# Optimization experiments

Hardware: AMD Instinct MI355X
Metric: run time of the kernel (lower is better)

Reference implementation:

```python
import jax, jax.numpy as jnp
import numpy as np

B, S, D, H, C, L, V, MLP, OUT = 2, 1024, 512, 8, 64, 1, 32000, 1024, 32000
DH = D // H
ROT = DH // 2  # RotaryEmbedding(dim=emb_dim//(2*n_heads)) -> rotates first d_head/2 dims
EPS = 1e-5
THETA = 10000.0


def layer_norm(x, g, b):
    m = x.mean(-1, keepdims=True)
    v = ((x - m) ** 2).mean(-1, keepdims=True)
    return (x - m) / jnp.sqrt(v + EPS) * g + b


def apply_rope(k):
    # k: (B, H, S, DH); interleaved-pair rotary on first ROT dims (rotary_embedding_torch)
    s = k.shape[-2]
    inv = 1.0 / (THETA ** (jnp.arange(0, ROT, 2, dtype=jnp.float32) / ROT))  # (ROT//2,)
    ang = jnp.arange(s, dtype=jnp.float32)[:, None] * inv[None, :]          # (S, ROT//2)
    ang = jnp.repeat(ang, 2, axis=-1)                                       # (S, ROT) interleaved
    cos, sin = jnp.cos(ang), jnp.sin(ang)
    kr = k[..., :ROT]
    k1, k2 = kr[..., 0::2], kr[..., 1::2]
    rot = jnp.stack([-k2, k1], axis=-1).reshape(kr.shape)
    kr = kr * cos + rot * sin
    return jnp.concatenate([kr, k[..., ROT:]], axis=-1)


def compression_attention(x, q_down, Wq, bq, Wk, bk, Wv, bv, Wo, bo):
    # x: (B, S, D) -- batch_first, causal branch, dropout=0 (eval)
    b_, s, d = x.shape
    qu = x @ Wq + bq
    kd = x @ Wk + bk
    vd = x @ Wv + bv
    vdk = vd @ Wk + bk
    vdv = vd @ Wv + bv
    split = lambda t: t.reshape(b_, s, H, DH).transpose(0, 2, 1, 3)  # (B,H,S,DH)
    qu, kd, vdk, vdv = map(split, (qu, kd, vdk, vdv))
    qd = q_down.reshape(C, H, DH).transpose(1, 0, 2)                 # (H,C,DH)
    kd = apply_rope(kd)
    scale = DH ** -0.5
    down = jnp.einsum('hcd,bhsd->bhcs', qd * scale, kd)              # (B,H,C,S)
    w = jnp.exp(down - down.max(-1, keepdims=True))
    norm = jnp.cumsum(w, axis=-1)                                    # (B,H,C,S)
    vkv = jnp.concatenate([vdk, vdv], axis=-1)                       # (B,H,S,2DH)
    # running compressed K/V state: (B,H,C,S,2DH)
    kvu = jnp.cumsum(w[..., None] * vkv[:, :, None, :, :], axis=3) / norm[..., None]
    ku, vu = kvu[..., :DH], kvu[..., DH:]
    up = jnp.einsum('bhsd,bhcsd->bhsc', qu * scale, ku)
    up = jax.nn.softmax(up, axis=-1)
    out = jnp.einsum('bhsc,bhcsd->bhsd', up, vu)
    out = out.transpose(0, 2, 1, 3).reshape(b_, s, d)
    return out @ Wo + bo


def setup_inputs():
    key = jax.random.key(0)
    ks = jax.random.split(key, 16)
    g = lambda i, shape, sc=0.02: jax.random.normal(ks[i], shape, jnp.float32) * sc
    return {
        'tokens': jax.random.randint(ks[0], (B, S), 0, V, dtype=jnp.int32),
        'emb': g(1, (V, D)),
        'ln1_g': jnp.ones((L, D), jnp.float32), 'ln1_b': jnp.zeros((L, D), jnp.float32),
        'q_down': g(2, (L, C, D)),
        'Wq': g(3, (L, D, D)), 'bq': jnp.zeros((L, D), jnp.float32),
        'Wk': g(4, (L, D, D)), 'bk': jnp.zeros((L, D), jnp.float32),
        'Wv': g(5, (L, D, D)), 'bv': jnp.zeros((L, D), jnp.float32),
        'Wo': g(6, (L, D, D)), 'bo': jnp.zeros((L, D), jnp.float32),
        'ln2_g': jnp.ones((L, D), jnp.float32), 'ln2_b': jnp.zeros((L, D), jnp.float32),
        'W1': g(7, (L, D, MLP)), 'b1': jnp.zeros((L, MLP), jnp.float32),
        'W2': g(8, (L, MLP, D)), 'b2': jnp.zeros((L, D), jnp.float32),
        'lnf_g': jnp.ones((D,), jnp.float32), 'lnf_b': jnp.zeros((D,), jnp.float32),
        'Wout': g(9, (D, OUT)),
    }


def reference(tokens, emb, ln1_g, ln1_b, q_down, Wq, bq, Wk, bk, Wv, bv, Wo, bo,
              ln2_g, ln2_b, W1, b1, W2, b2, lnf_g, lnf_b, Wout):
    x = emb[tokens]  # (B,S,D)
    for l in range(L):
        h = layer_norm(x, ln1_g[l], ln1_b[l])
        a = compression_attention(h, q_down[l], Wq[l], bq[l], Wk[l], bk[l],
                                  Wv[l], bv[l], Wo[l], bo[l])
        # NOTE: original code residual-adds to the *normed* x (x was reassigned)
        x = layer_norm(h + a, ln2_g[l], ln2_b[l])
        ff = jax.nn.relu(x @ W1[l] + b1[l]) @ W2[l] + b2[l]
        x = x + ff
    x = layer_norm(x, lnf_g, lnf_b)
    return x @ Wout  # (B,S,OUT)
```

## Files before the change

### kernel.cpp

```cpp
#include <hip/hip_runtime.h>
#include <hip/hip_bf16.h>
#include <cstdint>

typedef unsigned short u16;
typedef unsigned int u32;
typedef __bf16 bf16_t;
typedef bf16_t bf16x8 __attribute__((ext_vector_type(8)));
typedef float f32x4 __attribute__((ext_vector_type(4)));

constexpr int Bn = 2, Sn = 1024, Dn = 512, Hn = 8, Cn = 64, DHn = 64, ROTn = 32;
constexpr int MLPn = 1024, OUTn = 32000;
constexpr int NCH = 32;
constexpr int CSs = Sn / NCH;
constexpr float SCALE = 0.125f;
constexpr float EPSf = 1e-5f;
constexpr int QKVW = 1536;
constexpr int KVW = 1024;

__device__ __forceinline__ u16 f2b(float x) {
  u32 u = __float_as_uint(x);
  u32 r = (u + 0x7FFFu + ((u >> 16) & 1u)) >> 16;
  return (u16)r;
}

__global__ __launch_bounds__(256) void embed_ln_kernel(
    const int* __restrict__ tokens, const float* __restrict__ emb,
    const float* __restrict__ g, const float* __restrict__ bb,
    float* __restrict__ out, u16* __restrict__ out16) {
  int row = blockIdx.x;
  int tid = threadIdx.x;
  int tok = tokens[row];
  const float* src = emb + (size_t)tok * Dn;
  __shared__ float red[256];
  float v0 = src[tid], v1 = src[tid + 256];
  red[tid] = v0 + v1;
  __syncthreads();
  for (int s = 128; s > 0; s >>= 1) { if (tid < s) red[tid] += red[tid + s]; __syncthreads(); }
  float mean = red[0] * (1.0f / Dn);
  __syncthreads();
  float d0 = v0 - mean, d1 = v1 - mean;
  red[tid] = d0 * d0 + d1 * d1;
  __syncthreads();
  for (int s = 128; s > 0; s >>= 1) { if (tid < s) red[tid] += red[tid + s]; __syncthreads(); }
  float rstd = rsqrtf(red[0] * (1.0f / Dn) + EPSf);
  float o0 = d0 * rstd * g[tid] + bb[tid];
  float o1 = d1 * rstd * g[tid + 256] + bb[tid + 256];
  float* dst = out + (size_t)row * Dn;
  dst[tid] = o0; dst[tid + 256] = o1;
  u16* dst16 = out16 + (size_t)row * Dn;
  dst16[tid] = f2b(o0); dst16[tid + 256] = f2b(o1);
}

__global__ __launch_bounds__(256) void ln_kernel(
    const float* __restrict__ x, const float* __restrict__ res,
    const float* __restrict__ g, const float* __restrict__ bb,
    float* __restrict__ out, u16* __restrict__ out16) {
  int row = blockIdx.x;
  int tid = threadIdx.x;
  const float* xr = x + (size_t)row * Dn;
  float v0 = xr[tid], v1 = xr[tid + 256];
  if (res) {
    const float* rr = res + (size_t)row * Dn;
    v0 += rr[tid]; v1 += rr[tid + 256];
  }
  __shared__ float red[256];
  red[tid] = v0 + v1;
  __syncthreads();
  for (int s = 128; s > 0; s >>= 1) { if (tid < s) red[tid] += red[tid + s]; __syncthreads(); }
  float mean = red[0] * (1.0f / Dn);
  __syncthreads();
  float d0 = v0 - mean, d1 = v1 - mean;
  red[tid] = d0 * d0 + d1 * d1;
  __syncthreads();
  for (int s = 128; s > 0; s >>= 1) { if (tid < s) red[tid] += red[tid + s]; __syncthreads(); }
  float rstd = rsqrtf(red[0] * (1.0f / Dn) + EPSf);
  float o0 = d0 * rstd * g[tid] + bb[tid];
  float o1 = d1 * rstd * g[tid + 256] + bb[tid + 256];
  float* dst = out + (size_t)row * Dn;
  dst[tid] = o0; dst[tid + 256] = o1;
  if (out16) {
    u16* dst16 = out16 + (size_t)row * Dn;
    dst16[tid] = f2b(o0); dst16[tid + 256] = f2b(o1);
  }
}

__global__ __launch_bounds__(256) void prep_weights_kernel(
    const float* __restrict__ Wq, const float* __restrict__ Wk,
    const float* __restrict__ Wv, const float* __restrict__ Wo,
    const float* __restrict__ W1, const float* __restrict__ W2,
    u16* __restrict__ WqkvT, u16* __restrict__ WoT,
    u16* __restrict__ W1T, u16* __restrict__ W2T,
    const float* __restrict__ bq, const float* __restrict__ bk,
    const float* __restrict__ bv, float* __restrict__ bqkv) {
  int bid = blockIdx.x;
  int t = threadIdx.x;
  if (bid == 512) {
    for (int i = t; i < 512; i += 256) {
      bqkv[i] = bq[i]; bqkv[512 + i] = bk[i]; bqkv[1024 + i] = bv[i];
    }
    return;
  }
  const float* W; u16* Wt; int K, N, tile, nbx;
  if (bid < 64)       { W = Wq; Wt = WqkvT;              K = 512;  N = 512;  tile = bid;       nbx = 8;  }
  else if (bid < 128) { W = Wk; Wt = WqkvT + 512 * 512;  K = 512;  N = 512;  tile = bid - 64;  nbx = 8;  }
  else if (bid < 192) { W = Wv; Wt = WqkvT + 1024 * 512; K = 512;  N = 512;  tile = bid - 128; nbx = 8;  }
  else if (bid < 256) { W = Wo; Wt = WoT;                K = 512;  N = 512;  tile = bid - 192; nbx = 8;  }
  else if (bid < 384) { W = W1; Wt = W1T;                K = 512;  N = 1024; tile = bid - 256; nbx = 16; }
  else                { W = W2; Wt = W2T;                K = 1024; N = 512;  tile = bid - 384; nbx = 8;  }
  int n0 = (tile % nbx) * 64, k0 = (tile / nbx) * 64;

  __shared__ float tilebuf[64][65];
  int kr = t >> 4;
  int nc = (t & 15) * 4;
#pragma unroll
  for (int i = 0; i < 4; i++) {
    float4 v = *(const float4*)(W + (size_t)(k0 + kr + i * 16) * N + n0 + nc);
    tilebuf[kr + i * 16][nc] = v.x; tilebuf[kr + i * 16][nc + 1] = v.y;
    tilebuf[kr + i * 16][nc + 2] = v.z; tilebuf[kr + i * 16][nc + 3] = v.w;
  }
  __syncthreads();
  int n = t >> 2;
  int kb = (t & 3) * 16;
  u16 tmp[16];
#pragma unroll
  for (int j = 0; j < 16; j++) tmp[j] = f2b(tilebuf[kb + j][n]);
  u16* dst = Wt + (size_t)(n0 + n) * K + k0 + kb;
  *(uint4*)dst = *(uint4*)tmp;
  *(uint4*)(dst + 8) = *(uint4*)(tmp + 8);
}

template <bool BIAS, bool RES, bool RELU, bool WR32, bool WR16>
__global__ __launch_bounds__(256) void gemm16_kernel(
    const u16* __restrict__ A, const u16* __restrict__ Bt,
    const float* __restrict__ bias, const float* __restrict__ res,
    float* __restrict__ C, u16* __restrict__ C16,
    int M, int N, int K, int lda, int ldc) {
  __shared__ char smem[32768];
  u16* As = (u16*)smem;
  u16* Bs = (u16*)(smem + 16384);
  const int tid = threadIdx.x;
  const int lane = tid & 63;
  const int wv = tid >> 6;
  const int wr = wv >> 1, wc = wv & 1;
  const int m0 = blockIdx.y * 128, n0 = blockIdx.x * 128;

  f32x4 acc[4][4];
#pragma unroll
  for (int i = 0; i < 4; i++)
#pragma unroll
    for (int j = 0; j < 4; j++)
#pragma unroll
      for (int e = 0; e < 4; e++) acc[i][j][e] = 0.0f;

  const int srow = tid >> 3;
  const int sslot = tid & 7;
  const int csw = sslot ^ (srow & 7);
  const int fr = lane & 15, kq = lane >> 4, sx = lane & 7;

  uint4 ar[4], br[4];
  const u16* Arow = A + (size_t)(m0 + srow) * lda + sslot * 8;
  const u16* Brow = Bt + (size_t)(n0 + srow) * K + sslot * 8;
#pragma unroll
  for (int i = 0; i < 4; i++) {
    ar[i] = *(const uint4*)(Arow + (size_t)(i * 32) * lda);
    br[i] = *(const uint4*)(Brow + (size_t)(i * 32) * K);
  }

  for (int kt = 0; kt < K; kt += 64) {
    __syncthreads();
#pragma unroll
    for (int i = 0; i < 4; i++) {
      *(uint4*)(As + (srow + i * 32) * 64 + csw * 8) = ar[i];
      *(uint4*)(Bs + (srow + i * 32) * 64 + csw * 8) = br[i];
    }
    __syncthreads();
    if (kt + 64 < K) {
#pragma unroll
      for (int i = 0; i < 4; i++) {
        ar[i] = *(const uint4*)(Arow + (size_t)(i * 32) * lda + (kt + 64));
        br[i] = *(const uint4*)(Brow + (size_t)(i * 32) * K + (kt + 64));
      }
    }
#pragma unroll
    for (int ks = 0; ks < 2; ks++) {
      bf16x8 af[4], bfr[4];
#pragma unroll
      for (int i = 0; i < 4; i++) {
        int rA = wr * 64 + i * 16 + fr;
        af[i] = *(const bf16x8*)(As + rA * 64 + (((ks * 4 + kq) ^ sx) * 8));
        int rB = wc * 64 + i * 16 + fr;
        bfr[i] = *(const bf16x8*)(Bs + rB * 64 + (((ks * 4 + kq) ^ sx) * 8));
      }
#pragma unroll
      for (int mi = 0; mi < 4; mi++)
#pragma unroll
        for (int ni = 0; ni < 4; ni++)
          acc[mi][ni] = __builtin_amdgcn_mfma_f32_16x16x32_bf16(bfr[ni], af[mi], acc[mi][ni], 0, 0, 0);
    }
  }

  constexpr int CST = 132;
  float* cst = (float*)smem;
  const int rl = lane & 15, cg = (lane >> 4) * 4;
  const int erow = tid >> 5;
  const int ecol = (tid & 31) * 4;
  __syncthreads();
#pragma unroll
  for (int mi = 0; mi < 4; mi++) {
#pragma unroll
    for (int ni = 0; ni < 4; ni++)
      *(f32x4*)&cst[(wr * 16 + rl) * CST + wc * 64 + ni * 16 + cg] = acc[mi][ni];
    __syncthreads();
#pragma unroll
    for (int it = 0; it < 4; it++) {
      int lrow = it * 8 + erow;
      int grow = m0 + mi * 16 + (lrow & 15) + (lrow >> 4) * 64;
      int gcol = n0 + ecol;
      size_t gbase = (size_t)grow * ldc + gcol;
      f32x4 v = *(f32x4*)&cst[lrow * CST + ecol];
      if (BIAS) {
        float4 b4 = *(const float4*)(bias + gcol);
        v[0] += b4.x; v[1] += b4.y; v[2] += b4.z; v[3] += b4.w;
      }
      if (RES) {
        float4 r4 = *(const float4*)(res + gbase);
        v[0] += r4.x; v[1] += r4.y; v[2] += r4.z; v[3] += r4.w;
      }
      if (RELU) {
        v[0] = fmaxf(v[0], 0.f); v[1] = fmaxf(v[1], 0.f);
        v[2] = fmaxf(v[2], 0.f); v[3] = fmaxf(v[3], 0.f);
      }
      if (WR32) *(f32x4*)(C + gbase) = v;
      if (WR16) {
        uint2 p;
        p.x = (u32)f2b(v[0]) | ((u32)f2b(v[1]) << 16);
        p.y = (u32)f2b(v[2]) | ((u32)f2b(v[3]) << 16);
        *(uint2*)(C16 + gbase) = p;
      }
    }
    __syncthreads();
  }
}

__global__ __launch_bounds__(256, 2) void gemm_logits_kernel(
    const u16* __restrict__ A, const float* __restrict__ W,
    float* __restrict__ C, int M, int N, int K, int nby) {
  __shared__ char smem[49152];
  u16* As = (u16*)smem;
  u16* Bs = (u16*)(smem + 16384);
  const int tid = threadIdx.x;
  const int lane = tid & 63;
  const int wvid = tid >> 6;
  const int per = gridDim.x >> 3;
  const int lbid = (blockIdx.x & 7) * per + (blockIdx.x >> 3);
  const int bx = lbid / nby, by = lbid % nby;
  const int m0 = by * 128, n0 = bx * 256;

  f32x4 acc[8][4];
#pragma unroll
  for (int i = 0; i < 8; i++)
#pragma unroll
    for (int j = 0; j < 4; j++)
#pragma unroll
      for (int e = 0; e < 4; e++) acc[i][j][e] = 0.0f;

  const int srow = tid >> 3;
  const int sslot = tid & 7;
  const int csw = sslot ^ (srow & 7);
  const int fr = lane & 15, kq = lane >> 4, sx = lane & 7;
  const u16* Arow = A + (size_t)(m0 + srow) * K + sslot * 8;
  const float* Wcol = W + n0 + tid;
  const int bswz = tid & 7;

  for (int kt = 0; kt < K; kt += 64) {
    uint4 ar[4];
#pragma unroll
    for (int i = 0; i < 4; i++)
      ar[i] = *(const uint4*)(Arow + (size_t)(i * 32) * K + kt);
    float wld[64];
#pragma unroll
    for (int i = 0; i < 8; i++) {
      const float* wp = Wcol + (size_t)(kt + i * 8) * N;
#pragma unroll
      for (int j = 0; j < 8; j++) wld[i * 8 + j] = wp[(size_t)j * N];
    }
    __syncthreads();
#pragma unroll
    for (int i = 0; i < 4; i++)
      *(uint4*)(As + (srow + i * 32) * 64 + csw * 8) = ar[i];
#pragma unroll
    for (int i = 0; i < 8; i++) {
      u16 pk[8];
#pragma unroll
      for (int j = 0; j < 8; j++) pk[j] = f2b(wld[i * 8 + j]);
      *(uint4*)(Bs + tid * 64 + ((i ^ bswz) * 8)) = *(uint4*)pk;
    }
    __syncthreads();
#pragma unroll
    for (int ks = 0; ks < 2; ks++) {
      bf16x8 bfr[4];
#pragma unroll
      for (int ni = 0; ni < 4; ni++) {
        int rB = wvid * 64 + ni * 16 + fr;
        bfr[ni] = *(const bf16x8*)(Bs + rB * 64 + (((ks * 4 + kq) ^ sx) * 8));
      }
#pragma unroll
      for (int mi = 0; mi < 8; mi++) {
        int rA = mi * 16 + fr;
        bf16x8 af = *(const bf16x8*)(As + rA * 64 + (((ks * 4 + kq) ^ sx) * 8));
#pragma unroll
        for (int ni = 0; ni < 4; ni++)
          acc[mi][ni] = __builtin_amdgcn_mfma_f32_16x16x32_bf16(bfr[ni], af, acc[mi][ni], 0, 0, 0);
      }
    }
  }

  constexpr int CSTW = 264;
  float* cst = (float*)smem;
  const int rl = lane & 15, cg = (lane >> 4) * 4;
  const int erow = tid >> 5;
  const int ec = (tid & 31) * 4;
#pragma unroll
  for (int rg = 0; rg < 4; rg++) {
    __syncthreads();
#pragma unroll
    for (int q = 0; q < 2; q++) {
      int mi = rg * 2 + q;
#pragma unroll
      for (int ni = 0; ni < 4; ni++)
        *(f32x4*)&cst[(q * 16 + rl) * CSTW + wvid * 64 + ni * 16 + cg] = acc[mi][ni];
    }
    __syncthreads();
#pragma unroll
    for (int it = 0; it < 4; it++) {
      int lrow = it * 8 + erow;
      size_t gbase = (size_t)(m0 + rg * 32 + lrow) * N + n0;
      f32x4 v0 = *(f32x4*)&cst[lrow * CSTW + ec];
      f32x4 v1 = *(f32x4*)&cst[lrow * CSTW + 128 + ec];
      __builtin_nontemporal_store(v0, (f32x4*)(C + gbase + ec));
      __builtin_nontemporal_store(v1, (f32x4*)(C + gbase + 128 + ec));
    }
  }
}

__global__ void rope_kernel(float* __restrict__ qkv) {
  int idx = blockIdx.x * blockDim.x + threadIdx.x;
  if (idx >= Bn * Sn * Hn * (ROTn / 2)) return;
  int i = idx & 15;
  int h = (idx >> 4) & (Hn - 1);
  int s = (idx >> 7) & (Sn - 1);
  int b = idx >> 17;
  float inv = powf(10000.0f, -(float)(2 * i) / (float)ROTn);
  float ang = (float)s * inv;
  float c = cosf(ang), sn = sinf(ang);
  float* p = qkv + (size_t)(b * Sn + s) * QKVW + 512 + h * DHn + 2 * i;
  float k1 = p[0], k2 = p[1];
  p[0] = k1 * c - k2 * sn;
  p[1] = k2 * c + k1 * sn;
}

__global__ __launch_bounds__(256) void down_w_kernel(
    const float* __restrict__ q_down, const float* __restrict__ qkv,
    float* __restrict__ w) {
  int bid = blockIdx.x;
  int c = bid % Cn;
  int h = (bid / Cn) % Hn;
  int b = bid / (Cn * Hn);
  int tid = threadIdx.x;
  __shared__ float qv[DHn];
  __shared__ float red[256];
  if (tid < DHn) qv[tid] = q_down[(size_t)c * Dn + h * DHn + tid] * SCALE;
  __syncthreads();
  float dn[4];
  float lmax = -1e30f;
  for (int it = 0; it < 4; it++) {
    int s = tid + it * 256;
    const float* kp = qkv + (size_t)(b * Sn + s) * QKVW + 512 + h * DHn;
    float acc = 0.f;
#pragma unroll
    for (int d = 0; d < DHn; d += 4) {
      float4 kv = *(const float4*)(kp + d);
      acc += qv[d] * kv.x + qv[d + 1] * kv.y + qv[d + 2] * kv.z + qv[d + 3] * kv.w;
    }
    dn[it] = acc;
    lmax = fmaxf(lmax, acc);
  }
  red[tid] = lmax;
  __syncthreads();
  for (int st = 128; st > 0; st >>= 1) { if (tid < st) red[tid] = fmaxf(red[tid], red[tid + st]); __syncthreads(); }
  float mx = red[0];
  float* wp = w + (size_t)bid * Sn;
  for (int it = 0; it < 4; it++) wp[tid + it * 256] = expf(dn[it] - mx);
}

__global__ __launch_bounds__(256) void chunk_sums_kernel(
    const float* __restrict__ w, const float* __restrict__ vkv,
    float* __restrict__ chunkT) {
  int bid = blockIdx.x;
  int ch = bid % NCH;
  int h = (bid / NCH) % Hn;
  int b = bid / (NCH * Hn);
  int tid = threadIdx.x;
  int s0 = ch * CSs;
  __shared__ float vch[CSs][128];
  __shared__ float wch[Cn][CSs + 1];
#pragma unroll
  for (int i = 0; i < 4; i++) {
    int v = tid + i * 256;
    int t = v >> 5, dv = v & 31;
    int col = (dv < 16) ? (h * DHn + dv * 4) : (512 + h * DHn + (dv - 16) * 4);
    *(float4*)&vch[t][dv * 4] = *(const float4*)(vkv + (size_t)(b * Sn + s0 + t) * KVW + col);
  }
  for (int v = tid; v < Cn * CSs; v += 256) {
    int cc = v >> 5, t = v & 31;
    wch[cc][t] = w[((size_t)((b * Hn + h) * Cn + cc)) * Sn + s0 + t];
  }
  __syncthreads();
  int c = tid & 63, q = tid >> 6;
  float acc[32] = {};
  float nsum = 0.f;
  for (int t = 0; t < CSs; t++) {
    float wv = wch[c][t];
    nsum += wv;
#pragma unroll
    for (int j = 0; j < 8; j++) {
      float4 vv = *(float4*)&vch[t][q * 32 + j * 4];
      acc[j * 4 + 0] += wv * vv.x; acc[j * 4 + 1] += wv * vv.y;
      acc[j * 4 + 2] += wv * vv.z; acc[j * 4 + 3] += wv * vv.w;
    }
  }
  float* dst = chunkT + ((size_t)(((b * Hn + h) * Cn + c) * NCH + ch)) * 132;
#pragma unroll
  for (int j = 0; j < 8; j++) {
    float4 o; o.x = acc[j*4]; o.y = acc[j*4+1]; o.z = acc[j*4+2]; o.w = acc[j*4+3];
    *(float4*)(dst + q * 32 + j * 4) = o;
  }
  if (q == 0) dst[128] = nsum;
}

__global__ void scan_chunks_kernel(float* __restrict__ chunkT) {
  int tid = threadIdx.x;
  if (tid >= 129) return;
  size_t base = (size_t)blockIdx.x * NCH * 132 + tid;
  float run = 0.f;
  for (int ch = 0; ch < NCH; ch++) {
    float v = chunkT[base + (size_t)ch * 132];
    chunkT[base + (size_t)ch * 132] = run;
    run += v;
  }
}

__global__ __launch_bounds__(256) void attn_scan_kernel(
    const float* __restrict__ w, const float* __restrict__ vkv,
    const float* __restrict__ qkv, const float* __restrict__ chunkT,
    u16* __restrict__ ao16) {
  int bid = blockIdx.x;
  int ch = bid % NCH;
  int h = (bid / NCH) % Hn;
  int b = bid / (NCH * Hn);
  int tid = threadIdx.x;
  int c = tid & 63, q = tid >> 6;
  int s0 = ch * CSs;

  __shared__ float vch[CSs][128];
  __shared__ float wch[CSs][Cn + 1];
  __shared__ float qch[CSs][DHn];
  __shared__ float red[Cn][2];
  __shared__ float mres[Cn][DHn + 1];

#pragma unroll
  for (int i = 0; i < 4; i++) {
    int v = tid + i * 256;
    int t = v >> 5, dv = v & 31;
    int col = (dv < 16) ? (h * DHn + dv * 4) : (512 + h * DHn + (dv - 16) * 4);
    *(float4*)&vch[t][dv * 4] = *(const float4*)(vkv + (size_t)(b * Sn + s0 + t) * KVW + col);
  }
  for (int v = tid; v < CSs * DHn; v += 256) {
    int t = v >> 6, d = v & 63;
    qch[t][d] = qkv[(size_t)(b * Sn + s0 + t) * QKVW + h * DHn + d];
  }
  for (int v = tid; v < Cn * CSs; v += 256) {
    int cc = v >> 5, t = v & 31;
    wch[t][cc] = w[((size_t)((b * Hn + h) * Cn + cc)) * Sn + s0 + t];
  }
  const float* pre = chunkT + ((size_t)(((b * Hn + h) * Cn + c) * NCH + ch)) * 132;
  float acc[32];
#pragma unroll
  for (int j = 0; j < 8; j++) {
    float4 vv = *(const float4*)(pre + q * 32 + j * 4);
    acc[j * 4 + 0] = vv.x; acc[j * 4 + 1] = vv.y; acc[j * 4 + 2] = vv.z; acc[j * 4 + 3] = vv.w;
  }
  float norm = pre[128];
  __syncthreads();

  for (int t = 0; t < CSs; t++) {
    float wv = wch[t][c];
    norm += wv;
#pragma unroll
    for (int j = 0; j < 8; j++) {
      float4 vv = *(const float4*)&vch[t][q * 32 + j * 4];
      acc[j * 4 + 0] += wv * vv.x; acc[j * 4 + 1] += wv * vv.y;
      acc[j * 4 + 2] += wv * vv.z; acc[j * 4 + 3] += wv * vv.w;
    }
    if (q < 2) {
      float pd = 0.f;
#pragma unroll
      for (int j = 0; j < 8; j++) {
        float4 qv = *(const float4*)&qch[t][q * 32 + j * 4];
        pd += qv.x * acc[j * 4] + qv.y * acc[j * 4 + 1] + qv.z * acc[j * 4 + 2] + qv.w * acc[j * 4 + 3];
      }
      red[c][q] = pd;
    }
    __syncthreads();
    float u = (red[c][0] + red[c][1]) * SCALE / norm;
    float mx = u;
#pragma unroll
    for (int m = 32; m >= 1; m >>= 1) mx = fmaxf(mx, __shfl_xor(mx, m));
    float e = expf(u - mx);
    float sm = e;
#pragma unroll
    for (int m = 32; m >= 1; m >>= 1) sm += __shfl_xor(sm, m);
    float pp = e / (sm * norm);
    if (q >= 2) {
#pragma unroll
      for (int j = 0; j < 32; j++) mres[c][(q - 2) * 32 + j] = pp * acc[j];
    }
    __syncthreads();
    if (tid < 64) {
      float o = 0.f;
#pragma unroll
      for (int cc = 0; cc < 64; cc++) o += mres[cc][tid];
      ao16[(size_t)(b * Sn + s0 + t) * Dn + h * DHn + tid] = f2b(o);
    }
  }
}

extern "C" void kernel_launch(void* const* d_in, const int* in_sizes, int n_in,
                              void* d_out, int out_size, void* d_ws, size_t ws_size,
                              hipStream_t stream) {
  (void)in_sizes; (void)n_in; (void)out_size; (void)ws_size;
  const int*   tokens = (const int*)d_in[0];
  const float* emb    = (const float*)d_in[1];
  const float* ln1_g  = (const float*)d_in[2];
  const float* ln1_b  = (const float*)d_in[3];
  const float* q_down = (const float*)d_in[4];
  const float* Wq     = (const float*)d_in[5];
  const float* bq     = (const float*)d_in[6];
  const float* Wk     = (const float*)d_in[7];
  const float* bk     = (const float*)d_in[8];
  const float* Wv     = (const float*)d_in[9];
  const float* bv     = (const float*)d_in[10];
  const float* Wo     = (const float*)d_in[11];
  const float* bo     = (const float*)d_in[12];
  const float* ln2_g  = (const float*)d_in[13];
  const float* ln2_b  = (const float*)d_in[14];
  const float* W1     = (const float*)d_in[15];
  const float* b1     = (const float*)d_in[16];
  const float* W2     = (const float*)d_in[17];
  const float* b2     = (const float*)d_in[18];
  const float* lnf_g  = (const float*)d_in[19];
  const float* lnf_b  = (const float*)d_in[20];
  const float* Wout   = (const float*)d_in[21];
  float* out = (float*)d_out;

  float* ws = (float*)d_ws;
  float* qkv   = ws;
  u16*   qkv16 = (u16*)(ws + 3145728);
  float* vkv   = ws + 3932160;
  float* w     = ws + 6029312;
  float* chunk = ws + 7077888;
  float* h     = ws + 11403264;
  u16*   h16   = (u16*)(ws + 12451840);
  u16*   ao16  = (u16*)(ws + 12976128);
  float* a     = ws + 13500416;
  float* x2    = ws + 14548992;
  u16*   x216  = (u16*)(ws + 15597568);
  u16*   ff116 = (u16*)(ws + 16121856);
  u16*   WqkvT = (u16*)(ws + 17170432);
  u16*   WoT   = (u16*)(ws + 17563648);
  u16*   W1T   = (u16*)(ws + 17694720);
  u16*   W2T   = (u16*)(ws + 17956864);
  float* bqkv  = chunk;
  u16*   vd16  = qkv16 + 1024;
  float* x3    = a;
  u16*   xf16  = ao16;
  float* lnf32 = x2;

  const int M = Bn * Sn;

  embed_ln_kernel<<<M, 256, 0, stream>>>(tokens, emb, ln1_g, ln1_b, h, h16);

  prep_weights_kernel<<<513, 256, 0, stream>>>(
      Wq, Wk, Wv, Wo, W1, W2, WqkvT, WoT, W1T, W2T, bq, bk, bv, bqkv);

  gemm16_kernel<true, false, false, true, true>
      <<<dim3(QKVW / 128, M / 128), 256, 0, stream>>>(
      h16, WqkvT, bqkv, nullptr, qkv, qkv16, M, QKVW, Dn, Dn, QKVW);

  rope_kernel<<<(Bn * Sn * Hn * (ROTn / 2) + 255) / 256, 256, 0, stream>>>(qkv);
  down_w_kernel<<<Bn * Hn * Cn, 256, 0, stream>>>(q_down, qkv, w);

  gemm16_kernel<true, false, false, true, false>
      <<<dim3(KVW / 128, M / 128), 256, 0, stream>>>(
      vd16, WqkvT + 512 * 512, bqkv + 512, nullptr, vkv, nullptr, M, KVW, Dn, QKVW, KVW);

  chunk_sums_kernel<<<Bn * Hn * NCH, 256, 0, stream>>>(w, vkv, chunk);
  scan_chunks_kernel<<<Bn * Hn * Cn, 192, 0, stream>>>(chunk);
  attn_scan_kernel<<<Bn * Hn * NCH, 256, 0, stream>>>(w, vkv, qkv, chunk, ao16);

  gemm16_kernel<true, false, false, true, false>
      <<<dim3(Dn / 128, M / 128), 256, 0, stream>>>(
      ao16, WoT, bo, nullptr, a, nullptr, M, Dn, Dn, Dn, Dn);

  ln_kernel<<<M, 256, 0, stream>>>(a, h, ln2_g, ln2_b, x2, x216);

  gemm16_kernel<true, false, true, false, true>
      <<<dim3(MLPn / 128, M / 128), 256, 0, stream>>>(
      x216, W1T, b1, nullptr, nullptr, ff116, M, MLPn, Dn, Dn, MLPn);
  gemm16_kernel<true, true, false, true, false>
      <<<dim3(Dn / 128, M / 128), 256, 0, stream>>>(
      ff116, W2T, b2, x2, x3, nullptr, M, Dn, MLPn, MLPn, Dn);

  ln_kernel<<<M, 256, 0, stream>>>(x3, nullptr, lnf_g, lnf_b, lnf32, xf16);

  gemm_logits_kernel<<<dim3((OUTn / 256) * (M / 128), 1), 256, 0, stream>>>(
      xf16, Wout, out, M, OUTn, Dn, M / 128);
}
```

Baseline: 434.6 us.

## Shrink logits GEMM K-tile to 32 with padded LDS rows

```diff
diff --git a/kernel.cpp b/kernel.cpp
--- a/kernel.cpp
+++ b/kernel.cpp
@@ -245,9 +245,10 @@
 __global__ __launch_bounds__(256, 2) void gemm_logits_kernel(
     const u16* __restrict__ A, const float* __restrict__ W,
     float* __restrict__ C, int M, int N, int K, int nby) {
-  __shared__ char smem[49152];
+  constexpr int BRS = 40;
+  __shared__ char smem[30720];
   u16* As = (u16*)smem;
-  u16* Bs = (u16*)(smem + 16384);
+  u16* Bs = (u16*)(smem + 10240);
   const int tid = threadIdx.x;
   const int lane = tid & 63;
   const int wvid = tid >> 6;
@@ -264,81 +265,62 @@
 #pragma unroll
       for (int e = 0; e < 4; e++) acc[i][j][e] = 0.0f;
 
-  const int srow = tid >> 3;
-  const int sslot = tid & 7;
-  const int csw = sslot ^ (srow & 7);
-  const int fr = lane & 15, kq = lane >> 4, sx = lane & 7;
-  const u16* Arow = A + (size_t)(m0 + srow) * K + sslot * 8;
+  const int arow = tid >> 1;
+  const int acb = (tid & 1) * 2;
+  const int fr = lane & 15, kq = lane >> 4;
+  const u16* Ag = A + (size_t)(m0 + arow) * K + acb * 8;
   const float* Wcol = W + n0 + tid;
-  const int bswz = tid & 7;
-
-  for (int kt = 0; kt < K; kt += 64) {
-    uint4 ar[4];
-#pragma unroll
-    for (int i = 0; i < 4; i++)
-      ar[i] = *(const uint4*)(Arow + (size_t)(i * 32) * K + kt);
-    float wld[64];
-#pragma unroll
-    for (int i = 0; i < 8; i++) {
+
+  for (int kt = 0; kt < K; kt += 32) {
+    uint4 a0 = *(const uint4*)(Ag + kt);
+    uint4 a1 = *(const uint4*)(Ag + kt + 8);
+    float wld[32];
+#pragma unroll
+    for (int i = 0; i < 4; i++) {
       const float* wp = Wcol + (size_t)(kt + i * 8) * N;
 #pragma unroll
       for (int j = 0; j < 8; j++) wld[i * 8 + j] = wp[(size_t)j * N];
     }
     __syncthreads();
-#pragma unroll
-    for (int i = 0; i < 4; i++)
-      *(uint4*)(As + (srow + i * 32) * 64 + csw * 8) = ar[i];
-#pragma unroll
-    for (int i = 0; i < 8; i++) {
+    *(uint4*)(As + arow * BRS + (acb + 0) * 8) = a0;
+    *(uint4*)(As + arow * BRS + (acb + 1) * 8) = a1;
+#pragma unroll
+    for (int i = 0; i < 4; i++) {
       u16 pk[8];
 #pragma unroll
       for (int j = 0; j < 8; j++) pk[j] = f2b(wld[i * 8 + j]);
-      *(uint4*)(Bs + tid * 64 + ((i ^ bswz) * 8)) = *(uint4*)pk;
-    }
-    __syncthreads();
-#pragma unroll
-    for (int ks = 0; ks < 2; ks++) {
-      bf16x8 bfr[4];
-#pragma unroll
-      for (int ni = 0; ni < 4; ni++) {
-        int rB = wvid * 64 + ni * 16 + fr;
-        bfr[ni] = *(const bf16x8*)(Bs + rB * 64 + (((ks * 4 + kq) ^ sx) * 8));
-      }
-#pragma unroll
-      for (int mi = 0; mi < 8; mi++) {
-        int rA = mi * 16 + fr;
-        bf16x8 af = *(const bf16x8*)(As + rA * 64 + (((ks * 4 + kq) ^ sx) * 8));
-#pragma unroll
-        for (int ni = 0; ni < 4; ni++)
-          acc[mi][ni] = __builtin_amdgcn_mfma_f32_16x16x32_bf16(bfr[ni], af, acc[mi][ni], 0, 0, 0);
-      }
-    }
-  }
-
-  constexpr int CSTW = 264;
+      *(uint4*)(Bs + tid * BRS + i * 8) = *(uint4*)pk;
+    }
+    __syncthreads();
+    bf16x8 bfr[4];
+#pragma unroll
+    for (int ni = 0; ni < 4; ni++)
+      bfr[ni] = *(const bf16x8*)(Bs + (wvid * 64 + ni * 16 + fr) * BRS + kq * 8);
+#pragma unroll
+    for (int mi = 0; mi < 8; mi++) {
+      bf16x8 af = *(const bf16x8*)(As + (mi * 16 + fr) * BRS + kq * 8);
+#pragma unroll
+      for (int ni = 0; ni < 4; ni++)
+        acc[mi][ni] = __builtin_amdgcn_mfma_f32_16x16x32_bf16(bfr[ni], af, acc[mi][ni], 0, 0, 0);
+    }
+  }
+
+  constexpr int CSTW = 260;
   float* cst = (float*)smem;
-  const int rl = lane & 15, cg = (lane >> 4) * 4;
-  const int erow = tid >> 5;
-  const int ec = (tid & 31) * 4;
-#pragma unroll
-  for (int rg = 0; rg < 4; rg++) {
-    __syncthreads();
-#pragma unroll
-    for (int q = 0; q < 2; q++) {
-      int mi = rg * 2 + q;
-#pragma unroll
-      for (int ni = 0; ni < 4; ni++)
-        *(f32x4*)&cst[(q * 16 + rl) * CSTW + wvid * 64 + ni * 16 + cg] = acc[mi][ni];
-    }
+  const int cg = (lane >> 4) * 4;
+#pragma unroll
+  for (int mi = 0; mi < 8; mi++) {
+    __syncthreads();
+#pragma unroll
+    for (int ni = 0; ni < 4; ni++)
+      *(f32x4*)&cst[fr * CSTW + wvid * 64 + ni * 16 + cg] = acc[mi][ni];
     __syncthreads();
 #pragma unroll
     for (int it = 0; it < 4; it++) {
-      int lrow = it * 8 + erow;
-      size_t gbase = (size_t)(m0 + rg * 32 + lrow) * N + n0;
-      f32x4 v0 = *(f32x4*)&cst[lrow * CSTW + ec];
-      f32x4 v1 = *(f32x4*)&cst[lrow * CSTW + 128 + ec];
-      __builtin_nontemporal_store(v0, (f32x4*)(C + gbase + ec));
-      __builtin_nontemporal_store(v1, (f32x4*)(C + gbase + 128 + ec));
+      int r = it * 4 + wvid;
+      size_t gbase = (size_t)(m0 + mi * 16 + r) * N + n0 + lane * 4;
+      f32x4 v = *(f32x4*)&cst[r * CSTW + lane * 4];
+      __builtin_nontemporal_store(v, (f32x4*)(C + gbase));
     }
   }
 }
```

Result: faster. 409.3 us (-5.8%).
